# Optimization experiments

Measured on AMD Instinct MI355X. Metric: run time of the kernel, lower is better.

Reference implementation:

```python
import jax, jax.numpy as jnp
import numpy as np

B, N, F_IN, H, OUT = 64, 1024, 195, 128, 64
K1, K2 = N // 2, N // 4  # ceil(0.5*N), ceil(0.5*K1)
EPS = 1e-5


def setup_inputs() -> dict:
    key = jax.random.key(0)
    ks = jax.random.split(key, 16)
    rn = lambda k, s: jax.random.normal(k, s, dtype=jnp.float32) * 0.1
    inp = {
        "input": jax.random.normal(ks[0], (B, N, F_IN), dtype=jnp.float32),
        # SAGEConv1 (195->128): lin_l (neighbors, w/ bias), lin_r (root, no bias)
        "W1l": rn(ks[1], (H, F_IN)), "b1l": jnp.zeros((H,), jnp.float32),
        "W1r": rn(ks[2], (H, F_IN)),
        # SAGPooling1 GNN = GraphConv(128->1): lin_rel (sum aggr, w/ bias), lin_root (no bias)
        "Wp1_rel": rn(ks[3], (1, H)), "bp1_rel": jnp.zeros((1,), jnp.float32),
        "Wp1_root": rn(ks[4], (1, H)),
        # SAGEConv2 (128->64)
        "W2l": rn(ks[5], (OUT, H)), "b2l": jnp.zeros((OUT,), jnp.float32),
        "W2r": rn(ks[6], (OUT, H)),
        # SAGPooling2 GNN = GraphConv(64->1)
        "Wp2_rel": rn(ks[7], (1, OUT)), "bp2_rel": jnp.zeros((1,), jnp.float32),
        "Wp2_root": rn(ks[8], (1, OUT)),
        # MLP head
        "fc1_w": rn(ks[9], (512, OUT)), "fc1_b": jnp.zeros((512,), jnp.float32),
        "bn1_g": jnp.ones((512,), jnp.float32), "bn1_b": jnp.zeros((512,), jnp.float32),
        "bn1_m": jnp.zeros((512,), jnp.float32), "bn1_v": jnp.ones((512,), jnp.float32),
        "fc2_w": rn(ks[10], (256, 512)), "fc2_b": jnp.zeros((256,), jnp.float32),
        "bn2_g": jnp.ones((256,), jnp.float32), "bn2_b": jnp.zeros((256,), jnp.float32),
        "bn2_m": jnp.zeros((256,), jnp.float32), "bn2_v": jnp.ones((256,), jnp.float32),
        "fc3_w": rn(ks[11], (2, 256)), "fc3_b": jnp.zeros((2,), jnp.float32),
    }
    return inp


def _corr_adj(x):
    # Pearson corrcoef over rows of x [B,N,F] -> boolean adjacency [B,N,N] (corr > 0.5)
    xc = x - x.mean(axis=-1, keepdims=True)
    cov = jnp.einsum("bnf,bmf->bnm", xc, xc)
    d = jnp.sqrt(jnp.clip(jnp.einsum("bnnf->bn", cov[..., None] * 0 + 0) + jnp.diagonal(cov, axis1=1, axis2=2), 1e-12))
    corr = cov / (d[:, :, None] * d[:, None, :])
    return (corr > 0.5).astype(x.dtype)  # symmetric, includes self-loops


def _sage(x, A, Wl, bl, Wr):
    # PyG SAGEConv: lin_l(mean_{j in N(i)} x_j) + lin_r(x_i)
    deg = A.sum(axis=-1, keepdims=True)
    agg = jnp.einsum("bnm,bmf->bnf", A, x) / jnp.maximum(deg, 1.0)
    return jnp.einsum("bnf,hf->bnh", agg, Wl) + bl + jnp.einsum("bnf,hf->bnh", x, Wr)


def _sagpool(x, A, Wrel, brel, Wroot, k):
    # score via GraphConv (sum aggr): lin_rel(sum_j x_j) + lin_root(x_i)
    agg = jnp.einsum("bnm,bmf->bnf", A, x)
    score = (jnp.einsum("bnf,of->bno", agg, Wrel) + brel
             + jnp.einsum("bnf,of->bno", x, Wroot))[..., 0]  # [B,N]
    top_s, idx = jax.lax.top_k(score, k)  # per-graph top-k nodes
    x_new = jnp.take_along_axis(x, idx[:, :, None], axis=1) * jnp.tanh(top_s)[:, :, None]
    A_new = jnp.take_along_axis(A, idx[:, :, None], axis=1)
    A_new = jnp.take_along_axis(A_new, idx[:, None, :], axis=2)
    return x_new, A_new


def _bn_eval(x, g, b, m, v):
    return g * (x - m) * jax.lax.rsqrt(v + EPS) + b


def reference(input, W1l, b1l, W1r, Wp1_rel, bp1_rel, Wp1_root,
              W2l, b2l, W2r, Wp2_rel, bp2_rel, Wp2_root,
              fc1_w, fc1_b, bn1_g, bn1_b, bn1_m, bn1_v,
              fc2_w, fc2_b, bn2_g, bn2_b, bn2_m, bn2_v,
              fc3_w, fc3_b):
    A = _corr_adj(input)                                   # [B,N,N]
    x = jax.nn.relu(_sage(input, A, W1l, b1l, W1r))        # [B,N,128]
    x, A = _sagpool(x, A, Wp1_rel, bp1_rel, Wp1_root, K1)  # [B,K1,128]
    x = jax.nn.relu(_sage(x, A, W2l, b2l, W2r))            # [B,K1,64]
    x, A = _sagpool(x, A, Wp2_rel, bp2_rel, Wp2_root, K2)  # [B,K2,64]
    x = x.mean(axis=1)                                     # global mean pool -> [B,64]
    x = _bn_eval(jax.nn.relu(x @ fc1_w.T + fc1_b), bn1_g, bn1_b, bn1_m, bn1_v)
    x = _bn_eval(jax.nn.relu(x @ fc2_w.T + fc2_b), bn2_g, bn2_b, bn2_m, bn2_v)
    x = x @ fc3_w.T + fc3_b
    return jax.nn.softmax(x, axis=1)
```

## Files before the change

kernel.cpp:

```cpp
#include <hip/hip_runtime.h>
#include <cstdint>


typedef __bf16 bf16x8 __attribute__((ext_vector_type(8)));
typedef float  floatx4 __attribute__((ext_vector_type(4)));

#define MFMA_BF16(a, b, c) __builtin_amdgcn_mfma_f32_16x16x32_bf16((a), (b), (c), 0, 0, 0)

static constexpr int BATCH = 64, NNODE = 1024, FIN = 195, FPAD = 224;
static constexpr int HD = 128, OD = 64, KP1 = 512, KP2 = 256;

static constexpr size_t OFF_GHI   = 0;
static constexpr size_t OFF_GLO   = 8388608;
static constexpr size_t OFF_A1B   = 16777216;
static constexpr size_t OFF_YR2   = 18874368;
static constexpr size_t OFF_X2    = 35651584;
static constexpr size_t OFF_XHI   = 0;
static constexpr size_t OFF_XLO   = 29360128;
static constexpr size_t OFF_ABITS = 58720256;
static constexpr size_t OFF_X1    = 67108864;
static constexpr size_t OFF_P1    = 100663296;
static constexpr size_t OFF_Q1    = OFF_P1 + 262144;
static constexpr size_t OFF_S1    = OFF_Q1 + 262144;
static constexpr size_t OFF_IDX1  = OFF_S1 + 262144;
static constexpr size_t OFF_GATE1 = OFF_IDX1 + 131072;
static constexpr size_t OFF_P2    = OFF_GATE1 + 131072;
static constexpr size_t OFF_Q2    = OFF_P2 + 131072;
static constexpr size_t OFF_S2    = OFF_Q2 + 131072;
static constexpr size_t OFF_IDX2  = OFF_S2 + 131072;
static constexpr size_t OFF_GATE2 = OFF_IDX2 + 65536;
static constexpr size_t OFF_W1HI  = OFF_GATE2 + 65536;
static constexpr size_t OFF_W1LO  = OFF_W1HI + 114688;
static constexpr size_t OFF_W2HI  = OFF_W1LO + 114688;
static constexpr size_t OFF_W2LO  = OFF_W2HI + 32768;
static constexpr size_t OFF_XHAT  = 102760448;
static constexpr size_t OFF_YR1   = 102760448;

__global__ __launch_bounds__(256) void prep_pack_kernel(
    const float* __restrict__ x, __bf16* __restrict__ xhi,
    __bf16* __restrict__ xlo, __bf16* __restrict__ xhat,
    const float* __restrict__ W1l, const float* __restrict__ W1r,
    __bf16* __restrict__ hi1, __bf16* __restrict__ lo1,
    const float* __restrict__ W2l, const float* __restrict__ W2r,
    __bf16* __restrict__ hi2, __bf16* __restrict__ lo2) {
  int bid = blockIdx.x;
  if (bid < 16384) {
    int row  = bid * 4 + (threadIdx.x >> 6);
    int lane = threadIdx.x & 63;
    const float* xr = x + (long)row * FIN;
    int k0 = lane * 4;
    float v[4];
#pragma unroll
    for (int i = 0; i < 4; ++i) v[i] = (k0 + i < FIN) ? xr[k0 + i] : 0.f;
    float s = v[0] + v[1] + v[2] + v[3];
#pragma unroll
    for (int o = 32; o; o >>= 1) s += __shfl_xor(s, o);
    float mean = s * (1.f / (float)FIN);
    float c[4], ss = 0.f;
#pragma unroll
    for (int i = 0; i < 4; ++i) {
      c[i] = (k0 + i < FIN) ? (v[i] - mean) : 0.f;
      ss += c[i] * c[i];
    }
#pragma unroll
    for (int o = 32; o; o >>= 1) ss += __shfl_xor(ss, o);
    float inv = rsqrtf(fmaxf(ss, 1e-12f));
    if (k0 < FPAD) {
      __bf16 hi4[4], lo4[4], hat4[4];
#pragma unroll
      for (int i = 0; i < 4; ++i) {
        float xv = (k0 + i < FIN) ? v[i] : 0.f;
        __bf16 h = (__bf16)xv;
        hi4[i] = h;
        lo4[i] = (__bf16)(xv - (float)h);
        hat4[i] = (__bf16)(c[i] * inv);
      }
      long base = (long)row * FPAD + k0;
      *(uint2*)&xhi[base]  = *(const uint2*)hi4;
      *(uint2*)&xlo[base]  = *(const uint2*)lo4;
      *(uint2*)&xhat[base] = *(const uint2*)hat4;
    }
  } else if (bid < 16384 + 224) {
    int idx = (bid - 16384) * 256 + threadIdx.x;
    int h = idx / FPAD, k = idx % FPAD;
    float v = 0.f;
    if (k < FIN) v = (h < HD) ? W1l[h * FIN + k] : W1r[(h - HD) * FIN + k];
    __bf16 a = (__bf16)v;
    hi1[idx] = a;
    lo1[idx] = (__bf16)(v - (float)a);
  } else {
    int idx = (bid - 16384 - 224) * 256 + threadIdx.x;
    int h = idx / HD, k = idx % HD;
    float v = (h < OD) ? W2l[h * HD + k] : W2r[(h - OD) * HD + k];
    __bf16 a = (__bf16)v;
    hi2[idx] = a;
    lo2[idx] = (__bf16)(v - (float)a);
  }
}

__global__ __launch_bounds__(256) void corr_kernel(
    const __bf16* __restrict__ xhat, unsigned short* __restrict__ Abits) {
  int bid = blockIdx.x;
  int xcd = bid & 7;
  int m = bid >> 3;
  int b = xcd + ((m & 7) << 3);
  int rem = m >> 3, bi = 0;
  while (rem >= 8 - bi) { rem -= 8 - bi; ++bi; }
  int bj = bi + rem;
  int i0 = bi * 128, j0 = bj * 128;
  const __bf16* Xb = xhat + (long)b * NNODE * FPAD;
  int lane = threadIdx.x & 63, wave = threadIdx.x >> 6;
  int wi = (wave >> 1) * 64, wj = (wave & 1) * 64;
  int lr = lane & 15, lk = (lane >> 4) * 8;
  const __bf16* ai = Xb + (long)(i0 + wi + lr) * FPAD + lk;
  const __bf16* bjp = Xb + (long)(j0 + wj + lr) * FPAD + lk;
  floatx4 zero = {0.f, 0.f, 0.f, 0.f};
  floatx4 acc[4][4];
#pragma unroll
  for (int i = 0; i < 4; ++i)
#pragma unroll
    for (int j = 0; j < 4; ++j) acc[i][j] = zero;
  for (int kk = 0; kk < 7; ++kk) {
    int k0 = kk * 32;
    bf16x8 af[4], bf[4];
#pragma unroll
    for (int t = 0; t < 4; ++t) {
      af[t] = *(const bf16x8*)(ai + (long)t * 16 * FPAD + k0);
      bf[t] = *(const bf16x8*)(bjp + (long)t * 16 * FPAD + k0);
    }
#pragma unroll
    for (int ti = 0; ti < 4; ++ti)
#pragma unroll
      for (int tj = 0; tj < 4; ++tj)
        acc[ti][tj] = MFMA_BF16(af[ti], bf[tj], acc[ti][tj]);
  }
#pragma unroll
  for (int ti = 0; ti < 4; ++ti)
#pragma unroll
    for (int tj = 0; tj < 4; ++tj) {
      floatx4 a = acc[ti][tj];
      unsigned long long m0 = __ballot(a[0] > 0.5f);
      unsigned long long m1 = __ballot(a[1] > 0.5f);
      unsigned long long m2 = __ballot(a[2] > 0.5f);
      unsigned long long m3 = __ballot(a[3] > 0.5f);
      if (lane < 16) {
        unsigned long long mm = (lane & 2) ? ((lane & 1) ? m3 : m2)
                                           : ((lane & 1) ? m1 : m0);
        unsigned short piece = (unsigned short)(mm >> ((lane >> 2) * 16));
        int grow = i0 + wi + ti * 16 + lane;
        int gcol = (j0 + wj + tj * 16) >> 4;
        Abits[((long)b * NNODE + grow) * 64 + gcol] = piece;
      }
    }
}

__global__ __launch_bounds__(256) void gemm_split_kernel(
    const __bf16* __restrict__ Ahi, const __bf16* __restrict__ Alo,
    const __bf16* __restrict__ Bhi, const __bf16* __restrict__ Blo,
    float* __restrict__ C, int K, int ldc, int mblocks,
    unsigned long long* __restrict__ A64, int ntrans) {
  if ((int)blockIdx.x >= mblocks) {
    int t = ((int)blockIdx.x - mblocks) * gridDim.y + blockIdx.y;
    if (t >= ntrans) return;
    int b = t / 28, pi = t % 28;
    int rem = pi, rb = 1;
    while (rem >= rb) { rem -= rb; ++rb; }
    int cb = rem;
    int wave = threadIdx.x >> 6, lane = threadIdx.x & 63;
    int dr = rb * 2 + (wave >> 1);
    int dc = cb * 2 + (wave & 1);
    long base = (long)b * NNODE;
    unsigned long long xv = A64[(base + dc * 64 + lane) * 16 + dr];
    const unsigned long long M1  = 0x5555555555555555ULL;
    const unsigned long long M2  = 0x3333333333333333ULL;
    const unsigned long long M4  = 0x0F0F0F0F0F0F0F0FULL;
    const unsigned long long M8  = 0x00FF00FF00FF00FFULL;
    const unsigned long long M16 = 0x0000FFFF0000FFFFULL;
    const unsigned long long M32 = 0x00000000FFFFFFFFULL;
#define TSTEP(Kk, M)                                                      \
    {                                                                     \
      unsigned long long y = __shfl_xor(xv, Kk);                          \
      xv = ((lane & Kk) == 0) ? ((xv & (M)) | ((y & (M)) << Kk))          \
                              : ((xv & ~(M)) | ((y & ~(M)) >> Kk));       \
    }
    TSTEP(1, M1) TSTEP(2, M2) TSTEP(4, M4) TSTEP(8, M8) TSTEP(16, M16) TSTEP(32, M32)
#undef TSTEP
    A64[(base + dr * 64 + lane) * 16 + dc] = xv;
    return;
  }
  long row0 = (long)blockIdx.x * 128;
  int col0 = blockIdx.y * 128;
  int lane = threadIdx.x & 63, wave = threadIdx.x >> 6;
  int wi = (wave >> 1) * 64, wj = (wave & 1) * 64;
  int lr = lane & 15, lk = (lane >> 4) * 8;
  const __bf16* pAh = Ahi + (row0 + wi + lr) * (long)K + lk;
  const __bf16* pAl = Alo + (row0 + wi + lr) * (long)K + lk;
  const __bf16* pBh = Bhi + (long)(col0 + wj + lr) * K + lk;
  const __bf16* pBl = Blo + (long)(col0 + wj + lr) * K + lk;
  floatx4 zero = {0.f, 0.f, 0.f, 0.f};
  floatx4 acc[4][4];
#pragma unroll
  for (int i = 0; i < 4; ++i)
#pragma unroll
    for (int j = 0; j < 4; ++j) acc[i][j] = zero;
  int nk = K >> 5;
  for (int kk = 0; kk < nk; ++kk) {
    int k0 = kk * 32;
    bf16x8 ah[4], al[4], bh[4], bl[4];
#pragma unroll
    for (int t = 0; t < 4; ++t) {
      ah[t] = *(const bf16x8*)(pAh + (long)t * 16 * K + k0);
      al[t] = *(const bf16x8*)(pAl + (long)t * 16 * K + k0);
      bh[t] = *(const bf16x8*)(pBh + (long)t * 16 * K + k0);
      bl[t] = *(const bf16x8*)(pBl + (long)t * 16 * K + k0);
    }
#pragma unroll
    for (int tj = 0; tj < 4; ++tj)
#pragma unroll
      for (int ti = 0; ti < 4; ++ti) {
        acc[ti][tj] = MFMA_BF16(ah[ti], bh[tj], acc[ti][tj]);
        acc[ti][tj] = MFMA_BF16(ah[ti], bl[tj], acc[ti][tj]);
        acc[ti][tj] = MFMA_BF16(al[ti], bh[tj], acc[ti][tj]);
      }
  }
#pragma unroll
  for (int ti = 0; ti < 4; ++ti)
#pragma unroll
    for (int tj = 0; tj < 4; ++tj)
#pragma unroll
      for (int rr = 0; rr < 4; ++rr) {
        long grow = row0 + wi + ti * 16 + (lane >> 4) * 4 + rr;
        int gcol = col0 + wj + tj * 16 + (lane & 15);
        C[grow * ldc + gcol] = acc[ti][tj][rr];
      }
}

__global__ __launch_bounds__(256) void sage1_kernel(
    const unsigned int* __restrict__ Abits32, const float* __restrict__ YR1,
    const float* __restrict__ b1l, const float* __restrict__ Wrel,
    const float* __restrict__ Wroot, float* __restrict__ x1,
    float* __restrict__ p1, float* __restrict__ q1) {
  int half = threadIdx.x >> 7;
  int node = blockIdx.x * 2 + half;
  int b = node >> 10;
  int h = threadIdx.x & 127;
  __shared__ int list[2][1024];
  __shared__ int s_deg[2];
  __shared__ float redp[2][2], redq[2][2];
  if (h < 32) {
    unsigned int word = Abits32[(long)node * 32 + h];
    int cnt = __popc(word);
    int off = cnt;
#pragma unroll
    for (int o = 1; o < 32; o <<= 1) {
      int v = __shfl_up(off, o);
      if (h >= o) off += v;
    }
    off -= cnt;
    if (h == 31) s_deg[half] = off + cnt;
    int basei = h * 32;
    while (word) {
      int t = __ffs(word) - 1;
      word &= word - 1;
      list[half][off++] = basei + t;
    }
  }
  __syncthreads();
  int deg = s_deg[half];
  long ybase = (long)(b << 10) * 256;
  float accv = 0.f;
  for (int d = 0; d < deg; ++d)
    accv += YR1[ybase + (long)list[half][d] * 256 + h];
  float R = YR1[(long)node * 256 + 128 + h];
  float v = accv / (float)(deg < 1 ? 1 : deg) + b1l[h] + R;
  v = fmaxf(v, 0.f);
  x1[(long)node * 128 + h] = v;
  float pv = v * Wrel[h], qv = v * Wroot[h];
#pragma unroll
  for (int o = 32; o; o >>= 1) { pv += __shfl_xor(pv, o); qv += __shfl_xor(qv, o); }
  int wv = h >> 6, lane = h & 63;
  if (lane == 0) { redp[half][wv] = pv; redq[half][wv] = qv; }
  __syncthreads();
  if (h == 0) {
    p1[node] = redp[half][0] + redp[half][1];
    q1[node] = redq[half][0] + redq[half][1];
  }
}

__global__ __launch_bounds__(256) void score_kernel(
    const unsigned int* __restrict__ bits32, const float* __restrict__ p,
    const float* __restrict__ q, const float* __restrict__ brel,
    float* __restrict__ score, int nwords, int rpb_shift) {
  int row = blockIdx.x * 4 + (threadIdx.x >> 6);
  int lane = threadIdx.x & 63;
  int b = row >> rpb_shift;
  const unsigned int* wptr = bits32 + (long)row * nwords;
  const float* pb = p + ((long)b << rpb_shift);
  float s = 0.f;
  if (lane < nwords) {
    unsigned int word = wptr[lane];
    while (word) {
      int t = __ffs(word) - 1;
      word &= word - 1;
      s += pb[lane * 32 + t];
    }
  }
#pragma unroll
  for (int o = 32; o; o >>= 1) s += __shfl_xor(s, o);
  if (lane == 0) score[row] = s + q[row] + brel[0];
}

__global__ void topk_kernel(const float* __restrict__ score, int n, int k,
                            int* __restrict__ idx_out, float* __restrict__ gate_out) {
  int b = blockIdx.x, tid = threadIdx.x;
  float s = score[b * n + tid];
  unsigned int fb = __float_as_uint(s);
  unsigned int key = (fb & 0x80000000u) ? ~fb : (fb | 0x80000000u);
  __shared__ int hist[256];
  __shared__ unsigned int sh_prefix;
  __shared__ int sh_target, cnt_gt, cnt_eq, outpos;
  if (tid == 0) { sh_prefix = 0; sh_target = k; cnt_gt = 0; cnt_eq = 0; outpos = 0; }
  for (int shift = 24; shift >= 0; shift -= 8) {
    if (tid < 256) hist[tid] = 0;
    __syncthreads();
    unsigned int prefix = sh_prefix;
    bool inset = (shift == 24) || ((key >> (shift + 8)) == (prefix >> (shift + 8)));
    if (inset) atomicAdd(&hist[(key >> shift) & 255], 1);
    __syncthreads();
    if (tid < 64) {
      int lane = tid;
      int bb0 = hist[255 - 4 * lane];
      int bb1 = hist[254 - 4 * lane];
      int bb2 = hist[253 - 4 * lane];
      int bb3 = hist[252 - 4 * lane];
      int c0 = bb0, c1 = c0 + bb1, c2 = c1 + bb2, c3 = c2 + bb3;
      int incl = c3;
#pragma unroll
      for (int o = 1; o < 64; o <<= 1) {
        int v = __shfl_up(incl, o);
        if (lane >= o) incl += v;
      }
      int excl = incl - c3;
      int target = sh_target;
      int cum[4] = {excl + c0, excl + c1, excl + c2, excl + c3};
      int prev = excl;
#pragma unroll
      for (int i = 0; i < 4; ++i) {
        if (cum[i] >= target && prev < target) {
          int bin = 255 - (4 * lane + i);
          sh_prefix = prefix | ((unsigned int)bin << shift);
          sh_target = target - prev;
        }
        prev = cum[i];
      }
    }
    __syncthreads();
  }
  unsigned int T = sh_prefix;
  if (key > T) atomicAdd(&cnt_gt, 1);
  __syncthreads();
  int E = k - cnt_gt;
  bool sel = (key > T);
  if (!sel && key == T) sel = (atomicAdd(&cnt_eq, 1) < E);
  if (sel) {
    int posn = atomicAdd(&outpos, 1);
    idx_out[b * k + posn] = tid;
    gate_out[b * k + posn] = tanhf(s);
  }
}

__global__ __launch_bounds__(256) void gather_kernel(
    const float* __restrict__ x1, const int* __restrict__ idx,
    const float* __restrict__ gate, __bf16* __restrict__ ghi,
    __bf16* __restrict__ glo, const unsigned int* __restrict__ Abits32,
    unsigned long long* __restrict__ A1bits) {
  int bid = blockIdx.x;
  if (bid < 16384) {
    long e = (long)bid * 256 + threadIdx.x;
    int h = (int)(e & 127);
    int i = (int)((e >> 7) & 511);
    int b = (int)(e >> 16);
    int srow = idx[(b << 9) + i];
    float v = x1[((long)(b << 10) + srow) * 128 + h] * gate[(b << 9) + i];
    __bf16 a = (__bf16)v;
    ghi[e] = a;
    glo[e] = (__bf16)(v - (float)a);
  } else {
    int gi = (bid - 16384) * 4 + (threadIdx.x >> 6);
    int lane = threadIdx.x & 63;
    int b = gi >> 9;
    int srow = idx[gi];
    const unsigned int* src = Abits32 + ((long)(b << 10) + srow) * 32;
    const int* idxb = idx + (b << 9);
#pragma unroll
    for (int t = 0; t < 8; ++t) {
      int cj = idxb[t * 64 + lane];
      int bit = (src[cj >> 5] >> (cj & 31)) & 1;
      unsigned long long m = __ballot(bit);
      if (lane == 0) A1bits[(long)gi * 8 + t] = m;
    }
  }
}

__global__ __launch_bounds__(256) void sage2_kernel(
    const unsigned int* __restrict__ A1b32, const float* __restrict__ YR2,
    const float* __restrict__ b2l, const float* __restrict__ Wrel,
    const float* __restrict__ Wroot, float* __restrict__ x2,
    float* __restrict__ p2, float* __restrict__ q2) {
  int qw = threadIdx.x >> 6;
  int row = blockIdx.x * 4 + qw;
  int b = row >> 9;
  int h = threadIdx.x & 63;
  __shared__ int list[4][512];
  __shared__ int s_deg[4];
  if (h < 16) {
    unsigned int word = A1b32[(long)row * 16 + h];
    int cnt = __popc(word);
    int off = cnt;
#pragma unroll
    for (int o = 1; o < 16; o <<= 1) {
      int v = __shfl_up(off, o);
      if (h >= o) off += v;
    }
    off -= cnt;
    if (h == 15) s_deg[qw] = off + cnt;
    int basei = h * 32;
    while (word) {
      int t = __ffs(word) - 1;
      word &= word - 1;
      list[qw][off++] = basei + t;
    }
  }
  __syncthreads();
  int deg = s_deg[qw];
  long ybase = (long)(b << 9) * 128;
  float accv = 0.f;
  for (int d = 0; d < deg; ++d)
    accv += YR2[ybase + (long)list[qw][d] * 128 + h];
  float R = YR2[(long)row * 128 + 64 + h];
  float v = fmaxf(accv / (float)(deg < 1 ? 1 : deg) + b2l[h] + R, 0.f);
  x2[(long)row * 64 + h] = v;
  float pv = v * Wrel[h], qv = v * Wroot[h];
#pragma unroll
  for (int o = 32; o; o >>= 1) { pv += __shfl_xor(pv, o); qv += __shfl_xor(qv, o); }
  if (h == 0) { p2[row] = pv; q2[row] = qv; }
}

__global__ __launch_bounds__(512) void head_kernel(
    const float* __restrict__ x2, const int* __restrict__ idx2,
    const float* __restrict__ gate2, const float* __restrict__ fc1_w,
    const float* __restrict__ fc1_b, const float* __restrict__ g1,
    const float* __restrict__ bb1, const float* __restrict__ m1,
    const float* __restrict__ v1, const float* __restrict__ fc2_w,
    const float* __restrict__ fc2_b, const float* __restrict__ g2,
    const float* __restrict__ bb2, const float* __restrict__ m2,
    const float* __restrict__ v2, const float* __restrict__ fc3_w,
    const float* __restrict__ fc3_b, float* __restrict__ out) {
  int b = blockIdx.x, tid = threadIdx.x;
  __shared__ float part[8][64];
  __shared__ float pooled[64];
  __shared__ float h1[512];
  __shared__ float h2[256];
  __shared__ float zz[2];
  int h = tid & 63, grp = tid >> 6;
  float s = 0.f;
  for (int i = grp * 32; i < grp * 32 + 32; ++i) {
    int si = idx2[(b << 8) + i];
    s += x2[((long)(b << 9) + si) * 64 + h] * gate2[(b << 8) + i];
  }
  part[grp][h] = s;
  __syncthreads();
  if (tid < 64) {
    float t = 0.f;
#pragma unroll
    for (int g = 0; g < 8; ++g) t += part[g][tid];
    pooled[tid] = t * (1.f / 256.f);
  }
  __syncthreads();
  {
    float z = fc1_b[tid];
    for (int j = 0; j < 64; ++j) z += pooled[j] * fc1_w[tid * 64 + j];
    z = fmaxf(z, 0.f);
    h1[tid] = g1[tid] * (z - m1[tid]) * rsqrtf(v1[tid] + 1e-5f) + bb1[tid];
  }
  __syncthreads();
  if (tid < 256) {
    float z = fc2_b[tid];
    for (int j = 0; j < 512; ++j) z += h1[j] * fc2_w[tid * 512 + j];
    z = fmaxf(z, 0.f);
    h2[tid] = g2[tid] * (z - m2[tid]) * rsqrtf(v2[tid] + 1e-5f) + bb2[tid];
  }
  __syncthreads();
  if (tid < 2) {
    float z = fc3_b[tid];
    for (int j = 0; j < 256; ++j) z += h2[j] * fc3_w[tid * 256 + j];
    zz[tid] = z;
  }
  __syncthreads();
  if (tid == 0) {
    float mx = fmaxf(zz[0], zz[1]);
    float e0 = expf(zz[0] - mx), e1 = expf(zz[1] - mx);
    float inv = 1.f / (e0 + e1);
    out[b * 2 + 0] = e0 * inv;
    out[b * 2 + 1] = e1 * inv;
  }
}

extern "C" void kernel_launch(void* const* d_in, const int* in_sizes, int n_in,
                              void* d_out, int out_size, void* d_ws, size_t ws_size,
                              hipStream_t stream) {
  (void)in_sizes; (void)n_in; (void)out_size; (void)ws_size;
  const float* input   = (const float*)d_in[0];
  const float* W1l     = (const float*)d_in[1];
  const float* b1l     = (const float*)d_in[2];
  const float* W1r     = (const float*)d_in[3];
  const float* Wp1_rel = (const float*)d_in[4];
  const float* bp1_rel = (const float*)d_in[5];
  const float* Wp1_root= (const float*)d_in[6];
  const float* W2l     = (const float*)d_in[7];
  const float* b2l     = (const float*)d_in[8];
  const float* W2r     = (const float*)d_in[9];
  const float* Wp2_rel = (const float*)d_in[10];
  const float* bp2_rel = (const float*)d_in[11];
  const float* Wp2_root= (const float*)d_in[12];
  const float* fc1_w   = (const float*)d_in[13];
  const float* fc1_b   = (const float*)d_in[14];
  const float* bn1_g   = (const float*)d_in[15];
  const float* bn1_b   = (const float*)d_in[16];
  const float* bn1_m   = (const float*)d_in[17];
  const float* bn1_v   = (const float*)d_in[18];
  const float* fc2_w   = (const float*)d_in[19];
  const float* fc2_b   = (const float*)d_in[20];
  const float* bn2_g   = (const float*)d_in[21];
  const float* bn2_b   = (const float*)d_in[22];
  const float* bn2_m   = (const float*)d_in[23];
  const float* bn2_v   = (const float*)d_in[24];
  const float* fc3_w   = (const float*)d_in[25];
  const float* fc3_b   = (const float*)d_in[26];

  char* ws = (char*)d_ws;
  __bf16* xhi   = (__bf16*)(ws + OFF_XHI);
  __bf16* xlo   = (__bf16*)(ws + OFF_XLO);
  __bf16* xhat  = (__bf16*)(ws + OFF_XHAT);
  unsigned short* Abits = (unsigned short*)(ws + OFF_ABITS);
  const unsigned int* Abits32 = (const unsigned int*)(ws + OFF_ABITS);
  unsigned long long* A64 = (unsigned long long*)(ws + OFF_ABITS);
  float* YR1    = (float*)(ws + OFF_YR1);
  float* x1     = (float*)(ws + OFF_X1);
  float* p1     = (float*)(ws + OFF_P1);
  float* q1     = (float*)(ws + OFF_Q1);
  float* s1     = (float*)(ws + OFF_S1);
  int*   idx1   = (int*)(ws + OFF_IDX1);
  float* gate1  = (float*)(ws + OFF_GATE1);
  float* p2     = (float*)(ws + OFF_P2);
  float* q2     = (float*)(ws + OFF_Q2);
  float* s2     = (float*)(ws + OFF_S2);
  int*   idx2   = (int*)(ws + OFF_IDX2);
  float* gate2  = (float*)(ws + OFF_GATE2);
  __bf16* w1hi  = (__bf16*)(ws + OFF_W1HI);
  __bf16* w1lo  = (__bf16*)(ws + OFF_W1LO);
  __bf16* w2hi  = (__bf16*)(ws + OFF_W2HI);
  __bf16* w2lo  = (__bf16*)(ws + OFF_W2LO);
  __bf16* ghi   = (__bf16*)(ws + OFF_GHI);
  __bf16* glo   = (__bf16*)(ws + OFF_GLO);
  unsigned long long* A1bits = (unsigned long long*)(ws + OFF_A1B);
  const unsigned int* A1b32  = (const unsigned int*)(ws + OFF_A1B);
  float* YR2    = (float*)(ws + OFF_YR2);
  float* x2     = (float*)(ws + OFF_X2);
  float* out    = (float*)d_out;

  prep_pack_kernel<<<16672, 256, 0, stream>>>(input, xhi, xlo, xhat,
                                              W1l, W1r, w1hi, w1lo,
                                              W2l, W2r, w2hi, w2lo);
  corr_kernel<<<2304, 256, 0, stream>>>(xhat, Abits);
  gemm_split_kernel<<<dim3(512 + 896, 2), 256, 0, stream>>>(
      xhi, xlo, w1hi, w1lo, YR1, 224, 256, 512, A64, 1792);
  sage1_kernel<<<32768, 256, 0, stream>>>(Abits32, YR1, b1l, Wp1_rel, Wp1_root, x1, p1, q1);
  score_kernel<<<16384, 256, 0, stream>>>(Abits32, p1, q1, bp1_rel, s1, 32, 10);
  topk_kernel<<<64, 1024, 0, stream>>>(s1, 1024, KP1, idx1, gate1);
  gather_kernel<<<24576, 256, 0, stream>>>(x1, idx1, gate1, ghi, glo, Abits32, A1bits);
  gemm_split_kernel<<<dim3(256, 1), 256, 0, stream>>>(
      ghi, glo, w2hi, w2lo, YR2, 128, 128, 256, nullptr, 0);
  sage2_kernel<<<8192, 256, 0, stream>>>(A1b32, YR2, b2l, Wp2_rel, Wp2_root, x2, p2, q2);
  score_kernel<<<8192, 256, 0, stream>>>(A1b32, p2, q2, bp2_rel, s2, 16, 9);
  topk_kernel<<<64, 512, 0, stream>>>(s2, 512, KP2, idx2, gate2);
  head_kernel<<<64, 512, 0, stream>>>(x2, idx2, gate2, fc1_w, fc1_b, bn1_g, bn1_b,
                                      bn1_m, bn1_v, fc2_w, fc2_b, bn2_g, bn2_b,
                                      bn2_m, bn2_v, fc3_w, fc3_b, out);
}
```

Before: 399.3 us.

## Stage corr tiles in LDS and template split GEMM with XCD-aware mapping

The correlation kernel now cooperatively loads each 128x32 i/j tile into padded shared memory, and all waves read their fragments from LDS instead of each wave doing strided global loads, cutting redundant global traffic. The split-precision GEMM is templated on K and column count, so the K loop fully unrolls with constant strides. It also switches to a 1D grid whose block-to-row mapping groups rows per XCD for L2 locality, with a launch bound of two blocks per CU. The cost is two extra barriers per K step in corr, and possible register pressure from the unrolling and occupancy hint.

Result: faster. 376.4 us (-5.7%).

```diff
diff --git a/kernel.cpp b/kernel.cpp
--- a/kernel.cpp
+++ b/kernel.cpp
@@ -98,8 +98,11 @@
   }
 }
 
+static constexpr int CK = 40;
 __global__ __launch_bounds__(256) void corr_kernel(
     const __bf16* __restrict__ xhat, unsigned short* __restrict__ Abits) {
+  __shared__ __align__(16) __bf16 sI[128 * CK];
+  __shared__ __align__(16) __bf16 sJ[128 * CK];
   int bid = blockIdx.x;
   int xcd = bid & 7;
   int m = bid >> 3;
@@ -112,8 +115,8 @@
   int lane = threadIdx.x & 63, wave = threadIdx.x >> 6;
   int wi = (wave >> 1) * 64, wj = (wave & 1) * 64;
   int lr = lane & 15, lk = (lane >> 4) * 8;
-  const __bf16* ai = Xb + (long)(i0 + wi + lr) * FPAD + lk;
-  const __bf16* bjp = Xb + (long)(j0 + wj + lr) * FPAD + lk;
+  int strow = threadIdx.x & 127;
+  int stc = (threadIdx.x >> 7) * 8;
   floatx4 zero = {0.f, 0.f, 0.f, 0.f};
   floatx4 acc[4][4];
 #pragma unroll
@@ -122,11 +125,21 @@
     for (int j = 0; j < 4; ++j) acc[i][j] = zero;
   for (int kk = 0; kk < 7; ++kk) {
     int k0 = kk * 32;
+    __syncthreads();
+    {
+      const __bf16* gI = Xb + (long)(i0 + strow) * FPAD + k0;
+      const __bf16* gJ = Xb + (long)(j0 + strow) * FPAD + k0;
+      *(uint4*)&sI[strow * CK + stc]      = *(const uint4*)(gI + stc);
+      *(uint4*)&sI[strow * CK + stc + 16] = *(const uint4*)(gI + stc + 16);
+      *(uint4*)&sJ[strow * CK + stc]      = *(const uint4*)(gJ + stc);
+      *(uint4*)&sJ[strow * CK + stc + 16] = *(const uint4*)(gJ + stc + 16);
+    }
+    __syncthreads();
     bf16x8 af[4], bf[4];
 #pragma unroll
     for (int t = 0; t < 4; ++t) {
-      af[t] = *(const bf16x8*)(ai + (long)t * 16 * FPAD + k0);
-      bf[t] = *(const bf16x8*)(bjp + (long)t * 16 * FPAD + k0);
+      af[t] = *(const bf16x8*)&sI[(wi + t * 16 + lr) * CK + lk];
+      bf[t] = *(const bf16x8*)&sJ[(wj + t * 16 + lr) * CK + lk];
     }
 #pragma unroll
     for (int ti = 0; ti < 4; ++ti)
@@ -154,13 +167,16 @@
     }
 }
 
-__global__ __launch_bounds__(256) void gemm_split_kernel(
+template <int K, int NCOL>
+__global__ __launch_bounds__(256, 2) void gemm_split_kernel(
     const __bf16* __restrict__ Ahi, const __bf16* __restrict__ Alo,
     const __bf16* __restrict__ Bhi, const __bf16* __restrict__ Blo,
-    float* __restrict__ C, int K, int ldc, int mblocks,
+    float* __restrict__ C, int mblocks,
     unsigned long long* __restrict__ A64, int ntrans) {
-  if ((int)blockIdx.x >= mblocks) {
-    int t = ((int)blockIdx.x - mblocks) * gridDim.y + blockIdx.y;
+  constexpr int ldc = NCOL * 128;
+  int bid = blockIdx.x;
+  if (bid >= mblocks * NCOL) {
+    int t = bid - mblocks * NCOL;
     if (t >= ntrans) return;
     int b = t / 28, pi = t % 28;
     int rem = pi, rb = 1;
@@ -188,8 +204,18 @@
     A64[(base + dr * 64 + lane) * 16 + dc] = xv;
     return;
   }
-  long row0 = (long)blockIdx.x * 128;
-  int col0 = blockIdx.y * 128;
+  int mrow, col;
+  if (NCOL == 2) {
+    int xcd = bid & 7;
+    int q = bid >> 3;
+    col = q & 1;
+    mrow = (xcd << 6) + (q >> 1);
+  } else {
+    mrow = bid;
+    col = 0;
+  }
+  long row0 = (long)mrow * 128;
+  int col0 = col * 128;
   int lane = threadIdx.x & 63, wave = threadIdx.x >> 6;
   int wi = (wave >> 1) * 64, wj = (wave & 1) * 64;
   int lr = lane & 15, lk = (lane >> 4) * 8;
@@ -203,8 +229,8 @@
   for (int i = 0; i < 4; ++i)
 #pragma unroll
     for (int j = 0; j < 4; ++j) acc[i][j] = zero;
-  int nk = K >> 5;
-  for (int kk = 0; kk < nk; ++kk) {
+#pragma unroll
+  for (int kk = 0; kk < (K >> 5); ++kk) {
     int k0 = kk * 32;
     bf16x8 ah[4], al[4], bh[4], bl[4];
 #pragma unroll
@@ -573,14 +599,14 @@
                                               W1l, W1r, w1hi, w1lo,
                                               W2l, W2r, w2hi, w2lo);
   corr_kernel<<<2304, 256, 0, stream>>>(xhat, Abits);
-  gemm_split_kernel<<<dim3(512 + 896, 2), 256, 0, stream>>>(
-      xhi, xlo, w1hi, w1lo, YR1, 224, 256, 512, A64, 1792);
+  gemm_split_kernel<224, 2><<<1024 + 1792, 256, 0, stream>>>(
+      xhi, xlo, w1hi, w1lo, YR1, 512, A64, 1792);
   sage1_kernel<<<32768, 256, 0, stream>>>(Abits32, YR1, b1l, Wp1_rel, Wp1_root, x1, p1, q1);
   score_kernel<<<16384, 256, 0, stream>>>(Abits32, p1, q1, bp1_rel, s1, 32, 10);
   topk_kernel<<<64, 1024, 0, stream>>>(s1, 1024, KP1, idx1, gate1);
   gather_kernel<<<24576, 256, 0, stream>>>(x1, idx1, gate1, ghi, glo, Abits32, A1bits);
-  gemm_split_kernel<<<dim3(256, 1), 256, 0, stream>>>(
-      ghi, glo, w2hi, w2lo, YR2, 128, 128, 256, nullptr, 0);
+  gemm_split_kernel<128, 1><<<256, 256, 0, stream>>>(
+      ghi, glo, w2hi, w2lo, YR2, 256, nullptr, 0);
   sage2_kernel<<<8192, 256, 0, stream>>>(A1b32, YR2, b2l, Wp2_rel, Wp2_root, x2, p2, q2);
   score_kernel<<<8192, 256, 0, stream>>>(A1b32, p2, q2, bp2_rel, s2, 16, 9);
   topk_kernel<<<64, 512, 0, stream>>>(s2, 512, KP2, idx2, gate2);
```
